# Kernel tuning notes

Measured on AMD Instinct MI355X. Metric: run time of the kernel, lower is better.

Reference implementation:

```python
import jax, jax.numpy as jnp
import numpy as np

B, N, D_IN, D_OUT = 16, 2048, 64, 64


def setup_inputs() -> dict:
    key = jax.random.key(0)
    k1, k2, k3, k4, k5 = jax.random.split(key, 5)
    x = jax.random.normal(k1, (B, N, D_IN), dtype=jnp.float32)
    weight = jax.random.normal(k2, (D_IN, D_OUT), dtype=jnp.float32) * (1.0 / np.sqrt(D_OUT))
    att = jax.random.uniform(k3, (N, N), dtype=jnp.float32, minval=-1.0 / np.sqrt(D_OUT), maxval=1.0 / np.sqrt(D_OUT))
    bias = jax.random.normal(k4, (D_OUT,), dtype=jnp.float32) * (1.0 / np.sqrt(D_OUT))
    mask = jax.random.randint(k5, (N, N), 0, 2, dtype=jnp.int32)
    return {"x": x, "weight": weight, "att": att, "bias": bias, "mask": mask}


def reference(x, weight, att, bias, mask):
    # x: [B, N, D_in]; weight: [D_in, D_out]; att, mask: [N, N]; bias: [D_out]
    support = jnp.einsum('bnd,de->bne', x, weight)          # [B, N, D_out]
    mup = jnp.einsum('bnd,bmd->bnm', x, x)                  # [B, N, N]
    norms = jnp.linalg.norm(x, axis=-1, keepdims=True)      # [B, N, 1]
    mdown = norms * jnp.swapaxes(norms, 1, 2)               # [B, N, N] outer product of norms
    w = mup / mdown                                         # cosine similarity
    adjacent = (att * mask.astype(jnp.float32)) * w         # masked attention * cosine weights
    out = jnp.einsum('bnm,bme->bne', adjacent, support)     # [B, N, D_out]
    return out + bias
```

## Files before the change

### kernel.cpp

```cpp
#include <hip/hip_runtime.h>
#include <stdint.h>

#define NN 2048

typedef short bf8_t __attribute__((ext_vector_type(8)));
typedef float f32x4 __attribute__((ext_vector_type(4)));

__device__ __forceinline__ unsigned int rbf(float f) {
    unsigned int u = __builtin_bit_cast(unsigned int, f);
    return u + 0x7FFFu + ((u >> 16) & 1u);
}
__device__ __forceinline__ unsigned short f2b(float f) { return (unsigned short)(rbf(f) >> 16); }
__device__ __forceinline__ unsigned int pk2(float lo, float hi) {
    return (rbf(lo) >> 16) | (rbf(hi) & 0xFFFF0000u);
}

__global__ __launch_bounds__(256) void prep_xsb(
    const float* __restrict__ x, const float* __restrict__ w,
    unsigned short* __restrict__ xB, unsigned short* __restrict__ sB)
{
    __shared__ unsigned short xs[64 * 72];
    __shared__ unsigned short xt[64 * 72];
    __shared__ unsigned short Wt[64 * 72];
    __shared__ unsigned short st[64 * 72];
    __shared__ float part[64][4];

    const int t = threadIdx.x;
    const int b = blockIdx.x >> 5, nt = blockIdx.x & 31;
    const int row = t >> 2, seg = t & 3;

    float4 xq[4], wq[4];
    const float* xp = x + ((size_t)(b * NN + nt * 64 + row)) * 64 + seg * 16;
    const float* wp = w + row * 64 + seg * 16;
    #pragma unroll
    for (int i = 0; i < 4; ++i) { xq[i] = ((const float4*)xp)[i]; wq[i] = ((const float4*)wp)[i]; }
    float ss = 0.f;
    #pragma unroll
    for (int i = 0; i < 4; ++i)
        ss += xq[i].x * xq[i].x + xq[i].y * xq[i].y + xq[i].z * xq[i].z + xq[i].w * xq[i].w;
    part[row][seg] = ss;
    #pragma unroll
    for (int i = 0; i < 4; ++i) {
        ((unsigned int*)&xs[row * 72 + seg * 16])[i * 2]     = pk2(xq[i].x, xq[i].y);
        ((unsigned int*)&xs[row * 72 + seg * 16])[i * 2 + 1] = pk2(xq[i].z, xq[i].w);
        Wt[(seg * 16 + i * 4 + 0) * 72 + row] = f2b(wq[i].x);
        Wt[(seg * 16 + i * 4 + 1) * 72 + row] = f2b(wq[i].y);
        Wt[(seg * 16 + i * 4 + 2) * 72 + row] = f2b(wq[i].z);
        Wt[(seg * 16 + i * 4 + 3) * 72 + row] = f2b(wq[i].w);
    }
    __syncthreads();

    const float rinv = 1.0f / sqrtf(part[row][0] + part[row][1] + part[row][2] + part[row][3]);
    #pragma unroll
    for (int i = 0; i < 4; ++i) {
        ((unsigned int*)&xt[row * 72 + seg * 16])[i * 2]     = pk2(xq[i].x * rinv, xq[i].y * rinv);
        ((unsigned int*)&xt[row * 72 + seg * 16])[i * 2 + 1] = pk2(xq[i].z * rinv, xq[i].w * rinv);
    }
    __syncthreads();

    const int wv = t >> 6, l = t & 63, c = l & 15, q = l >> 4;
    {
        bf8_t h0 = *(const bf8_t*)&xt[(wv * 16 + c) * 72 + q * 8];
        bf8_t h1 = *(const bf8_t*)&xt[(wv * 16 + c) * 72 + 32 + q * 8];
        unsigned short* base = xB + ((size_t)(b * 32 + nt)) * 4096 + wv * 1024 + l * 8;
        *(bf8_t*)base = h0;
        *(bf8_t*)(base + 512) = h1;
    }
    {
        bf8_t a0 = *(const bf8_t*)&xs[(wv * 16 + c) * 72 + q * 8];
        bf8_t a1 = *(const bf8_t*)&xs[(wv * 16 + c) * 72 + 32 + q * 8];
        #pragma unroll
        for (int cb = 0; cb < 4; ++cb) {
            bf8_t b0 = *(const bf8_t*)&Wt[(cb * 16 + c) * 72 + q * 8];
            bf8_t b1 = *(const bf8_t*)&Wt[(cb * 16 + c) * 72 + 32 + q * 8];
            f32x4 z = (f32x4){0.f, 0.f, 0.f, 0.f};
            z = __builtin_amdgcn_mfma_f32_16x16x32_bf16(a0, b0, z, 0, 0, 0);
            z = __builtin_amdgcn_mfma_f32_16x16x32_bf16(a1, b1, z, 0, 0, 0);
            #pragma unroll
            for (int r = 0; r < 4; ++r)
                st[(cb * 16 + c) * 72 + wv * 16 + q * 4 + r] = f2b(z[r]);
        }
    }
    __syncthreads();

    {
        bf8_t h0 = *(const bf8_t*)&st[(wv * 16 + c) * 72 + q * 8];
        bf8_t h1 = *(const bf8_t*)&st[(wv * 16 + c) * 72 + 32 + q * 8];
        unsigned short* base = sB + ((size_t)(b * 32 + nt)) * 4096 + wv * 1024 + l * 8;
        *(bf8_t*)base = h0;
        *(bf8_t*)(base + 512) = h1;
    }
}

__global__ __launch_bounds__(256) void prep_am(
    const float* __restrict__ att, const int* __restrict__ mask,
    unsigned short* __restrict__ amB)
{
    __shared__ unsigned short amt[64 * 72];
    const int t = threadIdx.x;
    const int it = blockIdx.x >> 5, mc = blockIdx.x & 31;
    const int row = t >> 2, seg = t & 3;
    const size_t g = ((size_t)(it * 64 + row)) * NN + mc * 64 + seg * 16;
    #pragma unroll
    for (int i = 0; i < 4; ++i) {
        float4 a = *(const float4*)(att + g + i * 4);
        int4   m = *(const int4*)(mask + g + i * 4);
        ((unsigned int*)&amt[row * 72 + seg * 16])[i * 2] =
            pk2(a.x * (float)m.x, a.y * (float)m.y);
        ((unsigned int*)&amt[row * 72 + seg * 16])[i * 2 + 1] =
            pk2(a.z * (float)m.z, a.w * (float)m.w);
    }
    __syncthreads();
    const int wv = t >> 6, l = t & 63, c = l & 15, q = l >> 4;
    unsigned int ww[8];
    #pragma unroll
    for (int rbi = 0; rbi < 4; ++rbi) {
        #pragma unroll
        for (int rp = 0; rp < 2; ++rp) {
            unsigned int lo = amt[(rbi * 16 + c) * 72 + wv * 16 + q * 4 + rp * 2];
            unsigned int hi = amt[(rbi * 16 + c) * 72 + wv * 16 + q * 4 + rp * 2 + 1];
            ww[rbi * 2 + rp] = lo | (hi << 16);
        }
    }
    unsigned short* base = amB + ((size_t)(it * 32 + mc)) * 4096 + wv * 1024 + l * 8;
    *(uint4*)base         = *(uint4*)&ww[0];
    *(uint4*)(base + 512) = *(uint4*)&ww[4];
}

__global__ __launch_bounds__(256, 2) void gcn_kernel(
    const unsigned short* __restrict__ xB, const unsigned short* __restrict__ sB,
    const unsigned short* __restrict__ amB, const float* __restrict__ bias,
    float* __restrict__ out)
{
    __shared__ unsigned short Adj[4][64 * 72];
    const int t = threadIdx.x;
    const int wm = t >> 6, l = t & 63, c = l & 15, q = l >> 4;
    const int b = blockIdx.x >> 5, it = blockIdx.x & 31;

    const unsigned short* xit = xB + ((size_t)(b * 32 + it)) * 4096;
    bf8_t xi0[4], xi1[4];
    #pragma unroll
    for (int rb = 0; rb < 4; ++rb) {
        xi0[rb] = *(const bf8_t*)(xit + rb * 1024 + l * 8);
        xi1[rb] = *(const bf8_t*)(xit + rb * 1024 + 512 + l * 8);
    }
    f32x4 acc[4][4];
    #pragma unroll
    for (int rb = 0; rb < 4; ++rb)
        #pragma unroll
        for (int cb = 0; cb < 4; ++cb) acc[rb][cb] = (f32x4){0.f, 0.f, 0.f, 0.f};

    unsigned short* adj = &Adj[wm][0];

    for (int tt = 0; tt < 8; ++tt) {
        const int mc = wm + tt * 4;
        const unsigned short* xmt = xB + ((size_t)(b * 32 + mc)) * 4096;
        const unsigned short* smt = sB + ((size_t)(b * 32 + mc)) * 4096;
        const unsigned short* amp = amB + ((size_t)(it * 32 + mc)) * 4096;
        bf8_t xm0[4], xm1[4], sm0[4], sm1[4];
        uint4 amv[8];
        #pragma unroll
        for (int cb = 0; cb < 4; ++cb) {
            xm0[cb] = *(const bf8_t*)(xmt + cb * 1024 + l * 8);
            xm1[cb] = *(const bf8_t*)(xmt + cb * 1024 + 512 + l * 8);
        }
        #pragma unroll
        for (int cb = 0; cb < 4; ++cb) {
            sm0[cb] = *(const bf8_t*)(smt + cb * 1024 + l * 8);
            sm1[cb] = *(const bf8_t*)(smt + cb * 1024 + 512 + l * 8);
        }
        #pragma unroll
        for (int j = 0; j < 8; ++j) amv[j] = *(const uint4*)(amp + j * 512 + l * 8);

        #pragma unroll
        for (int cbm = 0; cbm < 4; ++cbm) {
            #pragma unroll
            for (int rbi = 0; rbi < 4; ++rbi) {
                f32x4 z = (f32x4){0.f, 0.f, 0.f, 0.f};
                z = __builtin_amdgcn_mfma_f32_16x16x32_bf16(xm0[cbm], xi0[rbi], z, 0, 0, 0);
                z = __builtin_amdgcn_mfma_f32_16x16x32_bf16(xm1[cbm], xi1[rbi], z, 0, 0, 0);
                const unsigned int w0 = ((const unsigned int*)&amv[cbm * 2 + (rbi >> 1)])[(rbi & 1) * 2 + 0];
                const unsigned int w1 = ((const unsigned int*)&amv[cbm * 2 + (rbi >> 1)])[(rbi & 1) * 2 + 1];
                const float a0f = __builtin_bit_cast(float, w0 << 16);
                const float a1f = __builtin_bit_cast(float, w0 & 0xFFFF0000u);
                const float a2f = __builtin_bit_cast(float, w1 << 16);
                const float a3f = __builtin_bit_cast(float, w1 & 0xFFFF0000u);
                uint2 p;
                p.x = pk2(z[0] * a0f, z[1] * a1f);
                p.y = pk2(z[2] * a2f, z[3] * a3f);
                *(uint2*)&adj[(rbi * 16 + c) * 72 + cbm * 16 + q * 4] = p;
            }
        }
        #pragma unroll
        for (int rb = 0; rb < 4; ++rb) {
            bf8_t p0 = *(const bf8_t*)&adj[(rb * 16 + c) * 72 + q * 8];
            bf8_t p1 = *(const bf8_t*)&adj[(rb * 16 + c) * 72 + 32 + q * 8];
            #pragma unroll
            for (int cb = 0; cb < 4; ++cb) {
                acc[rb][cb] = __builtin_amdgcn_mfma_f32_16x16x32_bf16(p0, sm0[cb], acc[rb][cb], 0, 0, 0);
                acc[rb][cb] = __builtin_amdgcn_mfma_f32_16x16x32_bf16(p1, sm1[cb], acc[rb][cb], 0, 0, 0);
            }
        }
    }

    float* red = (float*)&Adj[0][0];
    const int i0 = it * 64;
    for (int h = 0; h < 2; ++h) {
        __syncthreads();
        #pragma unroll
        for (int rb2 = 0; rb2 < 2; ++rb2) {
            const int rb = h * 2 + rb2;
            #pragma unroll
            for (int cb = 0; cb < 4; ++cb)
                #pragma unroll
                for (int r = 0; r < 4; ++r)
                    red[wm * 2176 + (rb2 * 16 + q * 4 + r) * 68 + cb * 16 + c] = acc[rb][cb][r];
        }
        __syncthreads();
        #pragma unroll
        for (int rnd = 0; rnd < 8; ++rnd) {
            const int idx = rnd * 256 + t;
            const int row = idx >> 6, col = idx & 63;
            const float s = red[0 * 2176 + row * 68 + col] + red[1 * 2176 + row * 68 + col]
                          + red[2 * 2176 + row * 68 + col] + red[3 * 2176 + row * 68 + col];
            out[((size_t)(b * NN + i0 + h * 32 + row)) * 64 + col] = s + bias[col];
        }
    }
}

extern "C" void kernel_launch(void* const* d_in, const int* in_sizes, int n_in,
                              void* d_out, int out_size, void* d_ws, size_t ws_size,
                              hipStream_t stream) {
    const float* x    = (const float*)d_in[0];
    const float* w    = (const float*)d_in[1];
    const float* att  = (const float*)d_in[2];
    const float* bias = (const float*)d_in[3];
    const int*   mask = (const int*)d_in[4];
    float* out = (float*)d_out;

    unsigned short* xB  = (unsigned short*)d_ws;
    unsigned short* sB  = xB + (size_t)2 * 1024 * 1024;
    unsigned short* amB = sB + (size_t)2 * 1024 * 1024;

    prep_xsb<<<dim3(512), dim3(256), 0, stream>>>(x, w, xB, sB);
    prep_am<<<dim3(1024), dim3(256), 0, stream>>>(att, mask, amB);
    gcn_kernel<<<dim3(512), dim3(256), 0, stream>>>(xB, sB, amB, bias, out);
}
```

Measured before the change: 123.5 us.

## Split GCN reduction over m into two halves, merge prep kernels, add reduce pass

The two prep kernels are merged into one launch that branches on block index. The main kernel now splits the m-dimension into two halves, doubling the grid from 512 to 1024 blocks so the GPU's compute units are better filled. Each half writes fp32 partial sums to workspace, and a new reduce kernel adds the two partials plus bias. The launch bound is raised to 3 blocks per CU, and the support-tile loads are moved after the first MFMA stage to ease register pressure. The cost is an extra kernel launch and an extra round trip of partial outputs through memory.

```diff
diff --git a/kernel.cpp b/kernel.cpp
--- a/kernel.cpp
+++ b/kernel.cpp
@@ -15,127 +15,125 @@
     return (rbf(lo) >> 16) | (rbf(hi) & 0xFFFF0000u);
 }
 
-__global__ __launch_bounds__(256) void prep_xsb(
+__global__ __launch_bounds__(256) void prep_kernel(
     const float* __restrict__ x, const float* __restrict__ w,
-    unsigned short* __restrict__ xB, unsigned short* __restrict__ sB)
-{
-    __shared__ unsigned short xs[64 * 72];
-    __shared__ unsigned short xt[64 * 72];
-    __shared__ unsigned short Wt[64 * 72];
-    __shared__ unsigned short st[64 * 72];
-    __shared__ float part[64][4];
-
-    const int t = threadIdx.x;
-    const int b = blockIdx.x >> 5, nt = blockIdx.x & 31;
-    const int row = t >> 2, seg = t & 3;
-
-    float4 xq[4], wq[4];
-    const float* xp = x + ((size_t)(b * NN + nt * 64 + row)) * 64 + seg * 16;
-    const float* wp = w + row * 64 + seg * 16;
-    #pragma unroll
-    for (int i = 0; i < 4; ++i) { xq[i] = ((const float4*)xp)[i]; wq[i] = ((const float4*)wp)[i]; }
-    float ss = 0.f;
-    #pragma unroll
-    for (int i = 0; i < 4; ++i)
-        ss += xq[i].x * xq[i].x + xq[i].y * xq[i].y + xq[i].z * xq[i].z + xq[i].w * xq[i].w;
-    part[row][seg] = ss;
-    #pragma unroll
-    for (int i = 0; i < 4; ++i) {
-        ((unsigned int*)&xs[row * 72 + seg * 16])[i * 2]     = pk2(xq[i].x, xq[i].y);
-        ((unsigned int*)&xs[row * 72 + seg * 16])[i * 2 + 1] = pk2(xq[i].z, xq[i].w);
-        Wt[(seg * 16 + i * 4 + 0) * 72 + row] = f2b(wq[i].x);
-        Wt[(seg * 16 + i * 4 + 1) * 72 + row] = f2b(wq[i].y);
-        Wt[(seg * 16 + i * 4 + 2) * 72 + row] = f2b(wq[i].z);
-        Wt[(seg * 16 + i * 4 + 3) * 72 + row] = f2b(wq[i].w);
-    }
-    __syncthreads();
-
-    const float rinv = 1.0f / sqrtf(part[row][0] + part[row][1] + part[row][2] + part[row][3]);
-    #pragma unroll
-    for (int i = 0; i < 4; ++i) {
-        ((unsigned int*)&xt[row * 72 + seg * 16])[i * 2]     = pk2(xq[i].x * rinv, xq[i].y * rinv);
-        ((unsigned int*)&xt[row * 72 + seg * 16])[i * 2 + 1] = pk2(xq[i].z * rinv, xq[i].w * rinv);
-    }
-    __syncthreads();
-
-    const int wv = t >> 6, l = t & 63, c = l & 15, q = l >> 4;
-    {
-        bf8_t h0 = *(const bf8_t*)&xt[(wv * 16 + c) * 72 + q * 8];
-        bf8_t h1 = *(const bf8_t*)&xt[(wv * 16 + c) * 72 + 32 + q * 8];
-        unsigned short* base = xB + ((size_t)(b * 32 + nt)) * 4096 + wv * 1024 + l * 8;
-        *(bf8_t*)base = h0;
-        *(bf8_t*)(base + 512) = h1;
-    }
-    {
-        bf8_t a0 = *(const bf8_t*)&xs[(wv * 16 + c) * 72 + q * 8];
-        bf8_t a1 = *(const bf8_t*)&xs[(wv * 16 + c) * 72 + 32 + q * 8];
-        #pragma unroll
-        for (int cb = 0; cb < 4; ++cb) {
-            bf8_t b0 = *(const bf8_t*)&Wt[(cb * 16 + c) * 72 + q * 8];
-            bf8_t b1 = *(const bf8_t*)&Wt[(cb * 16 + c) * 72 + 32 + q * 8];
-            f32x4 z = (f32x4){0.f, 0.f, 0.f, 0.f};
-            z = __builtin_amdgcn_mfma_f32_16x16x32_bf16(a0, b0, z, 0, 0, 0);
-            z = __builtin_amdgcn_mfma_f32_16x16x32_bf16(a1, b1, z, 0, 0, 0);
-            #pragma unroll
-            for (int r = 0; r < 4; ++r)
-                st[(cb * 16 + c) * 72 + wv * 16 + q * 4 + r] = f2b(z[r]);
-        }
-    }
-    __syncthreads();
-
-    {
-        bf8_t h0 = *(const bf8_t*)&st[(wv * 16 + c) * 72 + q * 8];
-        bf8_t h1 = *(const bf8_t*)&st[(wv * 16 + c) * 72 + 32 + q * 8];
-        unsigned short* base = sB + ((size_t)(b * 32 + nt)) * 4096 + wv * 1024 + l * 8;
-        *(bf8_t*)base = h0;
-        *(bf8_t*)(base + 512) = h1;
-    }
-}
-
-__global__ __launch_bounds__(256) void prep_am(
     const float* __restrict__ att, const int* __restrict__ mask,
+    unsigned short* __restrict__ xB, unsigned short* __restrict__ sB,
     unsigned short* __restrict__ amB)
 {
-    __shared__ unsigned short amt[64 * 72];
+    __shared__ unsigned short lds[4 * 64 * 72];
+    __shared__ float part[64][4];
+
     const int t = threadIdx.x;
-    const int it = blockIdx.x >> 5, mc = blockIdx.x & 31;
     const int row = t >> 2, seg = t & 3;
-    const size_t g = ((size_t)(it * 64 + row)) * NN + mc * 64 + seg * 16;
-    #pragma unroll
-    for (int i = 0; i < 4; ++i) {
-        float4 a = *(const float4*)(att + g + i * 4);
-        int4   m = *(const int4*)(mask + g + i * 4);
-        ((unsigned int*)&amt[row * 72 + seg * 16])[i * 2] =
-            pk2(a.x * (float)m.x, a.y * (float)m.y);
-        ((unsigned int*)&amt[row * 72 + seg * 16])[i * 2 + 1] =
-            pk2(a.z * (float)m.z, a.w * (float)m.w);
-    }
-    __syncthreads();
     const int wv = t >> 6, l = t & 63, c = l & 15, q = l >> 4;
-    unsigned int ww[8];
-    #pragma unroll
-    for (int rbi = 0; rbi < 4; ++rbi) {
-        #pragma unroll
-        for (int rp = 0; rp < 2; ++rp) {
-            unsigned int lo = amt[(rbi * 16 + c) * 72 + wv * 16 + q * 4 + rp * 2];
-            unsigned int hi = amt[(rbi * 16 + c) * 72 + wv * 16 + q * 4 + rp * 2 + 1];
-            ww[rbi * 2 + rp] = lo | (hi << 16);
-        }
-    }
-    unsigned short* base = amB + ((size_t)(it * 32 + mc)) * 4096 + wv * 1024 + l * 8;
-    *(uint4*)base         = *(uint4*)&ww[0];
-    *(uint4*)(base + 512) = *(uint4*)&ww[4];
-}
-
-__global__ __launch_bounds__(256, 2) void gcn_kernel(
+
+    if (blockIdx.x < 512) {
+        unsigned short* xs = lds;
+        unsigned short* xt = lds + 4608;
+        unsigned short* Wt = lds + 9216;
+        unsigned short* st = lds + 13824;
+        const int b = blockIdx.x >> 5, nt = blockIdx.x & 31;
+
+        float4 xq[4], wq[4];
+        const float* xp = x + ((size_t)(b * NN + nt * 64 + row)) * 64 + seg * 16;
+        const float* wp = w + row * 64 + seg * 16;
+        #pragma unroll
+        for (int i = 0; i < 4; ++i) { xq[i] = ((const float4*)xp)[i]; wq[i] = ((const float4*)wp)[i]; }
+        float ss = 0.f;
+        #pragma unroll
+        for (int i = 0; i < 4; ++i)
+            ss += xq[i].x * xq[i].x + xq[i].y * xq[i].y + xq[i].z * xq[i].z + xq[i].w * xq[i].w;
+        part[row][seg] = ss;
+        #pragma unroll
+        for (int i = 0; i < 4; ++i) {
+            ((unsigned int*)&xs[row * 72 + seg * 16])[i * 2]     = pk2(xq[i].x, xq[i].y);
+            ((unsigned int*)&xs[row * 72 + seg * 16])[i * 2 + 1] = pk2(xq[i].z, xq[i].w);
+            Wt[(seg * 16 + i * 4 + 0) * 72 + row] = f2b(wq[i].x);
+            Wt[(seg * 16 + i * 4 + 1) * 72 + row] = f2b(wq[i].y);
+            Wt[(seg * 16 + i * 4 + 2) * 72 + row] = f2b(wq[i].z);
+            Wt[(seg * 16 + i * 4 + 3) * 72 + row] = f2b(wq[i].w);
+        }
+        __syncthreads();
+
+        const float rinv = 1.0f / sqrtf(part[row][0] + part[row][1] + part[row][2] + part[row][3]);
+        #pragma unroll
+        for (int i = 0; i < 4; ++i) {
+            ((unsigned int*)&xt[row * 72 + seg * 16])[i * 2]     = pk2(xq[i].x * rinv, xq[i].y * rinv);
+            ((unsigned int*)&xt[row * 72 + seg * 16])[i * 2 + 1] = pk2(xq[i].z * rinv, xq[i].w * rinv);
+        }
+        __syncthreads();
+
+        {
+            bf8_t h0 = *(const bf8_t*)&xt[(wv * 16 + c) * 72 + q * 8];
+            bf8_t h1 = *(const bf8_t*)&xt[(wv * 16 + c) * 72 + 32 + q * 8];
+            unsigned short* base = xB + ((size_t)(b * 32 + nt)) * 4096 + wv * 1024 + l * 8;
+            *(bf8_t*)base = h0;
+            *(bf8_t*)(base + 512) = h1;
+        }
+        {
+            bf8_t a0 = *(const bf8_t*)&xs[(wv * 16 + c) * 72 + q * 8];
+            bf8_t a1 = *(const bf8_t*)&xs[(wv * 16 + c) * 72 + 32 + q * 8];
+            #pragma unroll
+            for (int cb = 0; cb < 4; ++cb) {
+                bf8_t b0 = *(const bf8_t*)&Wt[(cb * 16 + c) * 72 + q * 8];
+                bf8_t b1 = *(const bf8_t*)&Wt[(cb * 16 + c) * 72 + 32 + q * 8];
+                f32x4 z = (f32x4){0.f, 0.f, 0.f, 0.f};
+                z = __builtin_amdgcn_mfma_f32_16x16x32_bf16(a0, b0, z, 0, 0, 0);
+                z = __builtin_amdgcn_mfma_f32_16x16x32_bf16(a1, b1, z, 0, 0, 0);
+                #pragma unroll
+                for (int r = 0; r < 4; ++r)
+                    st[(cb * 16 + c) * 72 + wv * 16 + q * 4 + r] = f2b(z[r]);
+            }
+        }
+        __syncthreads();
+        {
+            bf8_t h0 = *(const bf8_t*)&st[(wv * 16 + c) * 72 + q * 8];
+            bf8_t h1 = *(const bf8_t*)&st[(wv * 16 + c) * 72 + 32 + q * 8];
+            unsigned short* base = sB + ((size_t)(b * 32 + nt)) * 4096 + wv * 1024 + l * 8;
+            *(bf8_t*)base = h0;
+            *(bf8_t*)(base + 512) = h1;
+        }
+    } else {
+        unsigned short* amt = lds;
+        const int bid = blockIdx.x - 512;
+        const int it = bid >> 5, mc = bid & 31;
+        const size_t g = ((size_t)(it * 64 + row)) * NN + mc * 64 + seg * 16;
+        #pragma unroll
+        for (int i = 0; i < 4; ++i) {
+            float4 a = *(const float4*)(att + g + i * 4);
+            int4   m = *(const int4*)(mask + g + i * 4);
+            ((unsigned int*)&amt[row * 72 + seg * 16])[i * 2] =
+                pk2(a.x * (float)m.x, a.y * (float)m.y);
+            ((unsigned int*)&amt[row * 72 + seg * 16])[i * 2 + 1] =
+                pk2(a.z * (float)m.z, a.w * (float)m.w);
+        }
+        __syncthreads();
+        unsigned int ww[8];
+        #pragma unroll
+        for (int rbi = 0; rbi < 4; ++rbi) {
+            #pragma unroll
+            for (int rp = 0; rp < 2; ++rp) {
+                unsigned int lo = amt[(rbi * 16 + c) * 72 + wv * 16 + q * 4 + rp * 2];
+                unsigned int hi = amt[(rbi * 16 + c) * 72 + wv * 16 + q * 4 + rp * 2 + 1];
+                ww[rbi * 2 + rp] = lo | (hi << 16);
+            }
+        }
+        unsigned short* base = amB + ((size_t)(it * 32 + mc)) * 4096 + wv * 1024 + l * 8;
+        *(uint4*)base         = *(uint4*)&ww[0];
+        *(uint4*)(base + 512) = *(uint4*)&ww[4];
+    }
+}
+
+__global__ __launch_bounds__(256, 3) void gcn_kernel(
     const unsigned short* __restrict__ xB, const unsigned short* __restrict__ sB,
-    const unsigned short* __restrict__ amB, const float* __restrict__ bias,
-    float* __restrict__ out)
+    const unsigned short* __restrict__ amB, float* __restrict__ pout)
 {
     __shared__ unsigned short Adj[4][64 * 72];
     const int t = threadIdx.x;
     const int wm = t >> 6, l = t & 63, c = l & 15, q = l >> 4;
-    const int b = blockIdx.x >> 5, it = blockIdx.x & 31;
+    const int blk = blockIdx.x;
+    const int half = blk & 1, it = (blk >> 1) & 31, b = blk >> 6;
 
     const unsigned short* xit = xB + ((size_t)(b * 32 + it)) * 4096;
     bf8_t xi0[4], xi1[4];
@@ -152,8 +150,8 @@
 
     unsigned short* adj = &Adj[wm][0];
 
-    for (int tt = 0; tt < 8; ++tt) {
-        const int mc = wm + tt * 4;
+    for (int tt = 0; tt < 4; ++tt) {
+        const int mc = half * 16 + wm + tt * 4;
         const unsigned short* xmt = xB + ((size_t)(b * 32 + mc)) * 4096;
         const unsigned short* smt = sB + ((size_t)(b * 32 + mc)) * 4096;
         const unsigned short* amp = amB + ((size_t)(it * 32 + mc)) * 4096;
@@ -163,11 +161,6 @@
         for (int cb = 0; cb < 4; ++cb) {
             xm0[cb] = *(const bf8_t*)(xmt + cb * 1024 + l * 8);
             xm1[cb] = *(const bf8_t*)(xmt + cb * 1024 + 512 + l * 8);
-        }
-        #pragma unroll
-        for (int cb = 0; cb < 4; ++cb) {
-            sm0[cb] = *(const bf8_t*)(smt + cb * 1024 + l * 8);
-            sm1[cb] = *(const bf8_t*)(smt + cb * 1024 + 512 + l * 8);
         }
         #pragma unroll
         for (int j = 0; j < 8; ++j) amv[j] = *(const uint4*)(amp + j * 512 + l * 8);
@@ -192,6 +185,11 @@
             }
         }
         #pragma unroll
+        for (int cb = 0; cb < 4; ++cb) {
+            sm0[cb] = *(const bf8_t*)(smt + cb * 1024 + l * 8);
+            sm1[cb] = *(const bf8_t*)(smt + cb * 1024 + 512 + l * 8);
+        }
+        #pragma unroll
         for (int rb = 0; rb < 4; ++rb) {
             bf8_t p0 = *(const bf8_t*)&adj[(rb * 16 + c) * 72 + q * 8];
             bf8_t p1 = *(const bf8_t*)&adj[(rb * 16 + c) * 72 + 32 + q * 8];
@@ -204,7 +202,7 @@
     }
 
     float* red = (float*)&Adj[0][0];
-    const int i0 = it * 64;
+    float* pw = pout + (size_t)blk * 4096;
     for (int h = 0; h < 2; ++h) {
         __syncthreads();
         #pragma unroll
@@ -221,11 +219,28 @@
         for (int rnd = 0; rnd < 8; ++rnd) {
             const int idx = rnd * 256 + t;
             const int row = idx >> 6, col = idx & 63;
-            const float s = red[0 * 2176 + row * 68 + col] + red[1 * 2176 + row * 68 + col]
-                          + red[2 * 2176 + row * 68 + col] + red[3 * 2176 + row * 68 + col];
-            out[((size_t)(b * NN + i0 + h * 32 + row)) * 64 + col] = s + bias[col];
-        }
-    }
+            pw[(h * 32 + row) * 64 + col] =
+                  red[0 * 2176 + row * 68 + col] + red[1 * 2176 + row * 68 + col]
+                + red[2 * 2176 + row * 68 + col] + red[3 * 2176 + row * 68 + col];
+        }
+    }
+}
+
+__global__ __launch_bounds__(256) void reduce_kernel(
+    const float* __restrict__ p, const float* __restrict__ bias,
+    float* __restrict__ out)
+{
+    const int j = (blockIdx.x * 256 + threadIdx.x) * 4;
+    const int tile = j >> 12, off = j & 4095;
+    const float4 a  = *(const float4*)(p + (size_t)tile * 8192 + off);
+    const float4 bq = *(const float4*)(p + (size_t)tile * 8192 + 4096 + off);
+    const float4 bs = *(const float4*)(bias + (j & 63));
+    float4 o;
+    o.x = a.x + bq.x + bs.x;
+    o.y = a.y + bq.y + bs.y;
+    o.z = a.z + bq.z + bs.z;
+    o.w = a.w + bq.w + bs.w;
+    *(float4*)(out + j) = o;
 }
 
 extern "C" void kernel_launch(void* const* d_in, const int* in_sizes, int n_in,
@@ -241,8 +256,9 @@
     unsigned short* xB  = (unsigned short*)d_ws;
     unsigned short* sB  = xB + (size_t)2 * 1024 * 1024;
     unsigned short* amB = sB + (size_t)2 * 1024 * 1024;
-
-    prep_xsb<<<dim3(512), dim3(256), 0, stream>>>(x, w, xB, sB);
-    prep_am<<<dim3(1024), dim3(256), 0, stream>>>(att, mask, amB);
-    gcn_kernel<<<dim3(512), dim3(256), 0, stream>>>(xB, sB, amB, bias, out);
-}
+    float* pout = (float*)(amB + (size_t)4 * 1024 * 1024);
+
+    prep_kernel<<<dim3(1536), dim3(256), 0, stream>>>(x, w, att, mask, xB, sB, amB);
+    gcn_kernel<<<dim3(1024), dim3(256), 0, stream>>>(xB, sB, amB, pout);
+    reduce_kernel<<<dim3(2048), dim3(256), 0, stream>>>(pout, bias, out);
+}
```

Measured after the change: 129.8 us. 1.05x slower.

## Merge prep kernels, remap gcn block order, and double-buffer xm tile loads

Applied to the files above, without the earlier changes.

Merges the two preprocessing kernels into one launch of 1536 blocks that branch on block index, removing a launch and letting both prep jobs run concurrently. In the main kernel, the row-tile index is permuted so that neighbouring blocks touch different att/mask tiles, which may change L2 locality. The x_m tile for the next iteration is now prefetched into alternating register buffers while the loop is fully unrolled. This raises register pressure, and the merged kernel's shared-memory footprint grows to the largest branch.

```diff
diff --git a/kernel.cpp b/kernel.cpp
--- a/kernel.cpp
+++ b/kernel.cpp
@@ -15,116 +15,114 @@
     return (rbf(lo) >> 16) | (rbf(hi) & 0xFFFF0000u);
 }
 
-__global__ __launch_bounds__(256) void prep_xsb(
+__global__ __launch_bounds__(256) void prep_kernel(
     const float* __restrict__ x, const float* __restrict__ w,
-    unsigned short* __restrict__ xB, unsigned short* __restrict__ sB)
-{
-    __shared__ unsigned short xs[64 * 72];
-    __shared__ unsigned short xt[64 * 72];
-    __shared__ unsigned short Wt[64 * 72];
-    __shared__ unsigned short st[64 * 72];
-    __shared__ float part[64][4];
-
-    const int t = threadIdx.x;
-    const int b = blockIdx.x >> 5, nt = blockIdx.x & 31;
-    const int row = t >> 2, seg = t & 3;
-
-    float4 xq[4], wq[4];
-    const float* xp = x + ((size_t)(b * NN + nt * 64 + row)) * 64 + seg * 16;
-    const float* wp = w + row * 64 + seg * 16;
-    #pragma unroll
-    for (int i = 0; i < 4; ++i) { xq[i] = ((const float4*)xp)[i]; wq[i] = ((const float4*)wp)[i]; }
-    float ss = 0.f;
-    #pragma unroll
-    for (int i = 0; i < 4; ++i)
-        ss += xq[i].x * xq[i].x + xq[i].y * xq[i].y + xq[i].z * xq[i].z + xq[i].w * xq[i].w;
-    part[row][seg] = ss;
-    #pragma unroll
-    for (int i = 0; i < 4; ++i) {
-        ((unsigned int*)&xs[row * 72 + seg * 16])[i * 2]     = pk2(xq[i].x, xq[i].y);
-        ((unsigned int*)&xs[row * 72 + seg * 16])[i * 2 + 1] = pk2(xq[i].z, xq[i].w);
-        Wt[(seg * 16 + i * 4 + 0) * 72 + row] = f2b(wq[i].x);
-        Wt[(seg * 16 + i * 4 + 1) * 72 + row] = f2b(wq[i].y);
-        Wt[(seg * 16 + i * 4 + 2) * 72 + row] = f2b(wq[i].z);
-        Wt[(seg * 16 + i * 4 + 3) * 72 + row] = f2b(wq[i].w);
-    }
-    __syncthreads();
-
-    const float rinv = 1.0f / sqrtf(part[row][0] + part[row][1] + part[row][2] + part[row][3]);
-    #pragma unroll
-    for (int i = 0; i < 4; ++i) {
-        ((unsigned int*)&xt[row * 72 + seg * 16])[i * 2]     = pk2(xq[i].x * rinv, xq[i].y * rinv);
-        ((unsigned int*)&xt[row * 72 + seg * 16])[i * 2 + 1] = pk2(xq[i].z * rinv, xq[i].w * rinv);
-    }
-    __syncthreads();
-
-    const int wv = t >> 6, l = t & 63, c = l & 15, q = l >> 4;
-    {
-        bf8_t h0 = *(const bf8_t*)&xt[(wv * 16 + c) * 72 + q * 8];
-        bf8_t h1 = *(const bf8_t*)&xt[(wv * 16 + c) * 72 + 32 + q * 8];
-        unsigned short* base = xB + ((size_t)(b * 32 + nt)) * 4096 + wv * 1024 + l * 8;
-        *(bf8_t*)base = h0;
-        *(bf8_t*)(base + 512) = h1;
-    }
-    {
-        bf8_t a0 = *(const bf8_t*)&xs[(wv * 16 + c) * 72 + q * 8];
-        bf8_t a1 = *(const bf8_t*)&xs[(wv * 16 + c) * 72 + 32 + q * 8];
-        #pragma unroll
-        for (int cb = 0; cb < 4; ++cb) {
-            bf8_t b0 = *(const bf8_t*)&Wt[(cb * 16 + c) * 72 + q * 8];
-            bf8_t b1 = *(const bf8_t*)&Wt[(cb * 16 + c) * 72 + 32 + q * 8];
-            f32x4 z = (f32x4){0.f, 0.f, 0.f, 0.f};
-            z = __builtin_amdgcn_mfma_f32_16x16x32_bf16(a0, b0, z, 0, 0, 0);
-            z = __builtin_amdgcn_mfma_f32_16x16x32_bf16(a1, b1, z, 0, 0, 0);
-            #pragma unroll
-            for (int r = 0; r < 4; ++r)
-                st[(cb * 16 + c) * 72 + wv * 16 + q * 4 + r] = f2b(z[r]);
-        }
-    }
-    __syncthreads();
-
-    {
-        bf8_t h0 = *(const bf8_t*)&st[(wv * 16 + c) * 72 + q * 8];
-        bf8_t h1 = *(const bf8_t*)&st[(wv * 16 + c) * 72 + 32 + q * 8];
-        unsigned short* base = sB + ((size_t)(b * 32 + nt)) * 4096 + wv * 1024 + l * 8;
-        *(bf8_t*)base = h0;
-        *(bf8_t*)(base + 512) = h1;
-    }
-}
-
-__global__ __launch_bounds__(256) void prep_am(
     const float* __restrict__ att, const int* __restrict__ mask,
+    unsigned short* __restrict__ xB, unsigned short* __restrict__ sB,
     unsigned short* __restrict__ amB)
 {
-    __shared__ unsigned short amt[64 * 72];
+    __shared__ unsigned short lds[4 * 64 * 72];
+    __shared__ float part[64][4];
+
     const int t = threadIdx.x;
-    const int it = blockIdx.x >> 5, mc = blockIdx.x & 31;
     const int row = t >> 2, seg = t & 3;
-    const size_t g = ((size_t)(it * 64 + row)) * NN + mc * 64 + seg * 16;
-    #pragma unroll
-    for (int i = 0; i < 4; ++i) {
-        float4 a = *(const float4*)(att + g + i * 4);
-        int4   m = *(const int4*)(mask + g + i * 4);
-        ((unsigned int*)&amt[row * 72 + seg * 16])[i * 2] =
-            pk2(a.x * (float)m.x, a.y * (float)m.y);
-        ((unsigned int*)&amt[row * 72 + seg * 16])[i * 2 + 1] =
-            pk2(a.z * (float)m.z, a.w * (float)m.w);
-    }
-    __syncthreads();
     const int wv = t >> 6, l = t & 63, c = l & 15, q = l >> 4;
-    unsigned int ww[8];
-    #pragma unroll
-    for (int rbi = 0; rbi < 4; ++rbi) {
-        #pragma unroll
-        for (int rp = 0; rp < 2; ++rp) {
-            unsigned int lo = amt[(rbi * 16 + c) * 72 + wv * 16 + q * 4 + rp * 2];
-            unsigned int hi = amt[(rbi * 16 + c) * 72 + wv * 16 + q * 4 + rp * 2 + 1];
-            ww[rbi * 2 + rp] = lo | (hi << 16);
-        }
-    }
-    unsigned short* base = amB + ((size_t)(it * 32 + mc)) * 4096 + wv * 1024 + l * 8;
-    *(uint4*)base         = *(uint4*)&ww[0];
-    *(uint4*)(base + 512) = *(uint4*)&ww[4];
+
+    if (blockIdx.x < 512) {
+        unsigned short* xs = lds;
+        unsigned short* xt = lds + 4608;
+        unsigned short* Wt = lds + 9216;
+        unsigned short* st = lds + 13824;
+        const int b = blockIdx.x >> 5, nt = blockIdx.x & 31;
+
+        float4 xq[4], wq[4];
+        const float* xp = x + ((size_t)(b * NN + nt * 64 + row)) * 64 + seg * 16;
+        const float* wp = w + row * 64 + seg * 16;
+        #pragma unroll
+        for (int i = 0; i < 4; ++i) { xq[i] = ((const float4*)xp)[i]; wq[i] = ((const float4*)wp)[i]; }
+        float ss = 0.f;
+        #pragma unroll
+        for (int i = 0; i < 4; ++i)
+            ss += xq[i].x * xq[i].x + xq[i].y * xq[i].y + xq[i].z * xq[i].z + xq[i].w * xq[i].w;
+        part[row][seg] = ss;
+        #pragma unroll
+        for (int i = 0; i < 4; ++i) {
+            ((unsigned int*)&xs[row * 72 + seg * 16])[i * 2]     = pk2(xq[i].x, xq[i].y);
+            ((unsigned int*)&xs[row * 72 + seg * 16])[i * 2 + 1] = pk2(xq[i].z, xq[i].w);
+            Wt[(seg * 16 + i * 4 + 0) * 72 + row] = f2b(wq[i].x);
+            Wt[(seg * 16 + i * 4 + 1) * 72 + row] = f2b(wq[i].y);
+            Wt[(seg * 16 + i * 4 + 2) * 72 + row] = f2b(wq[i].z);
+            Wt[(seg * 16 + i * 4 + 3) * 72 + row] = f2b(wq[i].w);
+        }
+        __syncthreads();
+
+        const float rinv = 1.0f / sqrtf(part[row][0] + part[row][1] + part[row][2] + part[row][3]);
+        #pragma unroll
+        for (int i = 0; i < 4; ++i) {
+            ((unsigned int*)&xt[row * 72 + seg * 16])[i * 2]     = pk2(xq[i].x * rinv, xq[i].y * rinv);
+            ((unsigned int*)&xt[row * 72 + seg * 16])[i * 2 + 1] = pk2(xq[i].z * rinv, xq[i].w * rinv);
+        }
+        __syncthreads();
+
+        {
+            bf8_t h0 = *(const bf8_t*)&xt[(wv * 16 + c) * 72 + q * 8];
+            bf8_t h1 = *(const bf8_t*)&xt[(wv * 16 + c) * 72 + 32 + q * 8];
+            unsigned short* base = xB + ((size_t)(b * 32 + nt)) * 4096 + wv * 1024 + l * 8;
+            *(bf8_t*)base = h0;
+            *(bf8_t*)(base + 512) = h1;
+        }
+        {
+            bf8_t a0 = *(const bf8_t*)&xs[(wv * 16 + c) * 72 + q * 8];
+            bf8_t a1 = *(const bf8_t*)&xs[(wv * 16 + c) * 72 + 32 + q * 8];
+            #pragma unroll
+            for (int cb = 0; cb < 4; ++cb) {
+                bf8_t b0 = *(const bf8_t*)&Wt[(cb * 16 + c) * 72 + q * 8];
+                bf8_t b1 = *(const bf8_t*)&Wt[(cb * 16 + c) * 72 + 32 + q * 8];
+                f32x4 z = (f32x4){0.f, 0.f, 0.f, 0.f};
+                z = __builtin_amdgcn_mfma_f32_16x16x32_bf16(a0, b0, z, 0, 0, 0);
+                z = __builtin_amdgcn_mfma_f32_16x16x32_bf16(a1, b1, z, 0, 0, 0);
+                #pragma unroll
+                for (int r = 0; r < 4; ++r)
+                    st[(cb * 16 + c) * 72 + wv * 16 + q * 4 + r] = f2b(z[r]);
+            }
+        }
+        __syncthreads();
+        {
+            bf8_t h0 = *(const bf8_t*)&st[(wv * 16 + c) * 72 + q * 8];
+            bf8_t h1 = *(const bf8_t*)&st[(wv * 16 + c) * 72 + 32 + q * 8];
+            unsigned short* base = sB + ((size_t)(b * 32 + nt)) * 4096 + wv * 1024 + l * 8;
+            *(bf8_t*)base = h0;
+            *(bf8_t*)(base + 512) = h1;
+        }
+    } else {
+        unsigned short* amt = lds;
+        const int bid = blockIdx.x - 512;
+        const int it = bid >> 5, mc = bid & 31;
+        const size_t g = ((size_t)(it * 64 + row)) * NN + mc * 64 + seg * 16;
+        #pragma unroll
+        for (int i = 0; i < 4; ++i) {
+            float4 a = *(const float4*)(att + g + i * 4);
+            int4   m = *(const int4*)(mask + g + i * 4);
+            ((unsigned int*)&amt[row * 72 + seg * 16])[i * 2] =
+                pk2(a.x * (float)m.x, a.y * (float)m.y);
+            ((unsigned int*)&amt[row * 72 + seg * 16])[i * 2 + 1] =
+                pk2(a.z * (float)m.z, a.w * (float)m.w);
+        }
+        __syncthreads();
+        unsigned int ww[8];
+        #pragma unroll
+        for (int rbi = 0; rbi < 4; ++rbi) {
+            #pragma unroll
+            for (int rp = 0; rp < 2; ++rp) {
+                unsigned int lo = amt[(rbi * 16 + c) * 72 + wv * 16 + q * 4 + rp * 2];
+                unsigned int hi = amt[(rbi * 16 + c) * 72 + wv * 16 + q * 4 + rp * 2 + 1];
+                ww[rbi * 2 + rp] = lo | (hi << 16);
+            }
+        }
+        unsigned short* base = amB + ((size_t)(it * 32 + mc)) * 4096 + wv * 1024 + l * 8;
+        *(uint4*)base         = *(uint4*)&ww[0];
+        *(uint4*)(base + 512) = *(uint4*)&ww[4];
+    }
 }
 
 __global__ __launch_bounds__(256, 2) void gcn_kernel(
@@ -135,7 +133,9 @@
     __shared__ unsigned short Adj[4][64 * 72];
     const int t = threadIdx.x;
     const int wm = t >> 6, l = t & 63, c = l & 15, q = l >> 4;
-    const int b = blockIdx.x >> 5, it = blockIdx.x & 31;
+    const int bid = blockIdx.x;
+    const int r8 = bid & 31, b = bid >> 5;
+    const int it = (r8 & 7) * 4 + (r8 >> 3);
 
     const unsigned short* xit = xB + ((size_t)(b * 32 + it)) * 4096;
     bf8_t xi0[4], xi1[4];
@@ -152,25 +152,48 @@
 
     unsigned short* adj = &Adj[wm][0];
 
+    bf8_t xmA0[4], xmA1[4], xmB0[4], xmB1[4];
+    {
+        const unsigned short* xmt = xB + ((size_t)(b * 32 + wm)) * 4096;
+        #pragma unroll
+        for (int cb = 0; cb < 4; ++cb) {
+            xmA0[cb] = *(const bf8_t*)(xmt + cb * 1024 + l * 8);
+            xmA1[cb] = *(const bf8_t*)(xmt + cb * 1024 + 512 + l * 8);
+        }
+    }
+
+    #pragma unroll
     for (int tt = 0; tt < 8; ++tt) {
         const int mc = wm + tt * 4;
-        const unsigned short* xmt = xB + ((size_t)(b * 32 + mc)) * 4096;
         const unsigned short* smt = sB + ((size_t)(b * 32 + mc)) * 4096;
         const unsigned short* amp = amB + ((size_t)(it * 32 + mc)) * 4096;
-        bf8_t xm0[4], xm1[4], sm0[4], sm1[4];
+        bf8_t sm0[4], sm1[4];
         uint4 amv[8];
         #pragma unroll
-        for (int cb = 0; cb < 4; ++cb) {
-            xm0[cb] = *(const bf8_t*)(xmt + cb * 1024 + l * 8);
-            xm1[cb] = *(const bf8_t*)(xmt + cb * 1024 + 512 + l * 8);
-        }
+        for (int j = 0; j < 8; ++j) amv[j] = *(const uint4*)(amp + j * 512 + l * 8);
         #pragma unroll
         for (int cb = 0; cb < 4; ++cb) {
             sm0[cb] = *(const bf8_t*)(smt + cb * 1024 + l * 8);
             sm1[cb] = *(const bf8_t*)(smt + cb * 1024 + 512 + l * 8);
         }
-        #pragma unroll
-        for (int j = 0; j < 8; ++j) amv[j] = *(const uint4*)(amp + j * 512 + l * 8);
+        if (tt < 7) {
+            const unsigned short* xmn = xB + ((size_t)(b * 32 + mc + 4)) * 4096;
+            if ((tt & 1) == 0) {
+                #pragma unroll
+                for (int cb = 0; cb < 4; ++cb) {
+                    xmB0[cb] = *(const bf8_t*)(xmn + cb * 1024 + l * 8);
+                    xmB1[cb] = *(const bf8_t*)(xmn + cb * 1024 + 512 + l * 8);
+                }
+            } else {
+                #pragma unroll
+                for (int cb = 0; cb < 4; ++cb) {
+                    xmA0[cb] = *(const bf8_t*)(xmn + cb * 1024 + l * 8);
+                    xmA1[cb] = *(const bf8_t*)(xmn + cb * 1024 + 512 + l * 8);
+                }
+            }
+        }
+        const bf8_t* xm0 = (tt & 1) ? xmB0 : xmA0;
+        const bf8_t* xm1 = (tt & 1) ? xmB1 : xmA1;
 
         #pragma unroll
         for (int cbm = 0; cbm < 4; ++cbm) {
@@ -242,7 +265,6 @@
     unsigned short* sB  = xB + (size_t)2 * 1024 * 1024;
     unsigned short* amB = sB + (size_t)2 * 1024 * 1024;
 
-    prep_xsb<<<dim3(512), dim3(256), 0, stream>>>(x, w, xB, sB);
-    prep_am<<<dim3(1024), dim3(256), 0, stream>>>(att, mask, amB);
+    prep_kernel<<<dim3(1536), dim3(256), 0, stream>>>(x, w, att, mask, xB, sB, amB);
     gcn_kernel<<<dim3(512), dim3(256), 0, stream>>>(xB, sB, amB, bias, out);
 }
```

After: 115.2 us. 6.7% less time.
